# Kernel tuning notes

Measured on AMD Instinct MI355X. Metric: run time of the kernel, lower is better.

The kernel has to match this reference:

```python
import jax, jax.numpy as jnp
import numpy as np

B, S, H, NH = 2, 2048, 1024, 4
DH = H // NH
EPS = 1e-6


def setup_inputs() -> dict:
    key = jax.random.key(0)
    ks = jax.random.split(key, 6)
    q = jax.random.normal(ks[0], (B, S, H), dtype=jnp.float32)
    k = jax.random.normal(ks[1], (B, S, H), dtype=jnp.float32)
    v = jax.random.normal(ks[2], (B, S, H), dtype=jnp.float32)
    # gate projections: Linear(3*H -> NH). Kernels are zero-init in the module;
    # use small random kernels so the projection path is exercised.
    igate_kernel = jax.random.normal(ks[3], (3 * H, NH), dtype=jnp.float32) * 0.02
    fgate_kernel = jax.random.normal(ks[4], (3 * H, NH), dtype=jnp.float32) * 0.02
    igate_bias = jax.random.normal(ks[5], (NH,), dtype=jnp.float32) * 0.1
    fgate_bias = jnp.linspace(3.0, 6.0, NH, dtype=jnp.float32)  # bias_linspace_initializer
    outnorm_scale = jnp.ones((H,), dtype=jnp.float32)  # MultiHeadLayerNorm scale, no bias
    return {"q": q, "k": k, "v": v,
            "igate_kernel": igate_kernel, "igate_bias": igate_bias,
            "fgate_kernel": fgate_kernel, "fgate_bias": fgate_bias,
            "outnorm_scale": outnorm_scale}


def _parallel_stabilized(qh, kh, vh, ig, fg):
    # qh,kh,vh: (B,NH,S,DH); ig,fg: (B,NH,S,1) gate preactivations
    log_fg = jax.nn.log_sigmoid(fg)                      # (B,NH,S,1)
    cs = jnp.cumsum(log_fg, axis=2)                      # cumulative log forget gates
    ltr = jnp.tril(jnp.ones((qh.shape[2], qh.shape[2]), dtype=bool))
    # log decay matrix: sum_{t=j+1}^{i} log f_t = cs[i] - cs[j], masked causal
    log_fg_mat = jnp.where(ltr, cs - jnp.swapaxes(cs, 2, 3), -jnp.inf)  # (B,NH,S,S)
    log_D = log_fg_mat + jnp.swapaxes(ig, 2, 3)          # add input gate per column
    max_log_D = jnp.max(log_D, axis=-1, keepdims=True)   # row-wise stabilizer
    D = jnp.exp(log_D - max_log_D)                       # (B,NH,S,S)
    qk = jnp.einsum("bhsd,bhtd->bhst", qh, kh) / jnp.sqrt(jnp.float32(DH))
    C = qk * D
    normalizer = jnp.maximum(jnp.abs(jnp.sum(C, axis=-1, keepdims=True)),
                             jnp.exp(-max_log_D))
    return jnp.einsum("bhst,bhtd->bhsd", C / (normalizer + EPS), vh)


def reference(q, k, v, igate_kernel, igate_bias, fgate_kernel, fgate_bias, outnorm_scale):
    Bq, Sq, Hq = q.shape
    x = jnp.concatenate([q, k, v], axis=-1)              # (B,S,3H)
    ig = (x @ igate_kernel + igate_bias)                 # (B,S,NH)
    fg = (x @ fgate_kernel + fgate_bias)
    ig = jnp.transpose(ig, (0, 2, 1))[..., None]         # (B,NH,S,1)
    fg = jnp.transpose(fg, (0, 2, 1))[..., None]
    qh = jnp.transpose(q.reshape(Bq, Sq, NH, DH), (0, 2, 1, 3))
    kh = jnp.transpose(k.reshape(Bq, Sq, NH, DH), (0, 2, 1, 3))
    vh = jnp.transpose(v.reshape(Bq, Sq, NH, DH), (0, 2, 1, 3))
    h = _parallel_stabilized(qh, kh, vh, ig, fg)         # (B,NH,S,DH)
    # MultiHeadLayerNorm: per-head layernorm over DH, scale only
    mean = jnp.mean(h, axis=-1, keepdims=True)
    var = jnp.mean((h - mean) ** 2, axis=-1, keepdims=True)
    h_norm = (h - mean) * jax.lax.rsqrt(var + 1e-5)
    h_norm = h_norm * outnorm_scale.reshape(1, NH, 1, DH)
    out = jnp.transpose(h_norm, (0, 2, 1, 3)).reshape(Bq, Sq, Hq)
    return out
```

## Files before the change

### kernel.cpp

```cpp
#include <hip/hip_runtime.h>
#include <hip/hip_bf16.h>


#define S_LEN 2048
#define DHD   256
#define NHEAD 4
#define BATCH 2
#define HID   1024
#define BH_CNT (BATCH*NHEAD)

typedef __attribute__((ext_vector_type(8))) short bf16x8;
typedef __attribute__((ext_vector_type(4))) short short4v;
typedef __attribute__((ext_vector_type(4))) float f32x4;

static __device__ __forceinline__ short f2b(float f) {
  __hip_bfloat16 h = __float2bfloat16(f);
  return *reinterpret_cast<short*>(&h);
}

static __device__ __forceinline__ bf16x8 pack8(f32x4 a, f32x4 b) {
  bf16x8 o;
  o[0]=f2b(a[0]); o[1]=f2b(a[1]); o[2]=f2b(a[2]); o[3]=f2b(a[3]);
  o[4]=f2b(b[0]); o[5]=f2b(b[1]); o[6]=f2b(b[2]); o[7]=f2b(b[3]);
  return o;
}

static __device__ __forceinline__ void gload16(const void* src, void* ldsdst) {
  __builtin_amdgcn_global_load_lds(
      (const __attribute__((address_space(1))) void*)src,
      (__attribute__((address_space(3))) void*)ldsdst, 16, 0, 0);
}

__global__ __launch_bounds__(256) void prep_kernel(
    const float* __restrict__ q, const float* __restrict__ k, const float* __restrict__ v,
    const float* __restrict__ wi, const float* __restrict__ wf,
    short* __restrict__ Kg, short* __restrict__ Vg,
    float* __restrict__ igA, float* __restrict__ fgA) {
  __shared__ short vt2[32][264];
  const int bx = blockIdx.x, t = threadIdx.x;
  if (bx < 768) {
    const int w = t >> 6, lane = t & 63;
    const int gw = bx*4 + w;
    const int seg = gw % 3;
    const int rg = gw / 3;
    const float* xp = (seg == 0) ? q : (seg == 1) ? k : v;
    const float* wip = wi + (long)seg*HID*NHEAD;
    const float* wfp = wf + (long)seg*HID*NHEAD;
    f32x4 ai[4], af[4];
#pragma unroll
    for (int r = 0; r < 4; r++) { ai[r] = f32x4{0,0,0,0}; af[r] = f32x4{0,0,0,0}; }
    for (int cb = 0; cb < HID; cb += 64) {
      const int c = cb + lane;
      const f32x4 wiv = *(const f32x4*)(wip + (long)c*NHEAD);
      const f32x4 wfv = *(const f32x4*)(wfp + (long)c*NHEAD);
#pragma unroll
      for (int r = 0; r < 4; r++) {
        const float x = xp[(long)(rg*4 + r)*HID + c];
        ai[r] += x * wiv;
        af[r] += x * wfv;
      }
    }
#pragma unroll
    for (int mk = 32; mk >= 1; mk >>= 1)
#pragma unroll
      for (int r = 0; r < 4; r++)
#pragma unroll
        for (int e = 0; e < 4; e++) {
          ai[r][e] += __shfl_xor(ai[r][e], mk);
          af[r][e] += __shfl_xor(af[r][e], mk);
        }
    if (lane == 0) {
#pragma unroll
      for (int r = 0; r < 4; r++) {
        const long row = rg*4 + r;
#pragma unroll
        for (int e = 0; e < 4; e++) {
          unsafeAtomicAdd(&igA[row*NHEAD + e], ai[r][e]);
          unsafeAtomicAdd(&fgA[row*NHEAD + e], af[r][e]);
        }
      }
    }
  } else if (bx < 2816) {
    const int kb = bx - 768;
    const int g_row = kb*2 + (t >> 7);
    const int col = (t & 127) * 8;
    const long off = (long)g_row*HID + col;
    const f32x4 xk0 = *(const f32x4*)(k + off);
    const f32x4 xk1 = *(const f32x4*)(k + off + 4);
    bf16x8 o = pack8(xk0, xk1);
    const int b = g_row >> 11, s = g_row & (S_LEN-1);
    const int hh = col >> 8, d = col & 255;
    const int bh = b*NHEAD + hh, jt = s >> 5, rr = s & 31;
    *(bf16x8*)(Kg + ((long)bh*64 + jt)*8192 + rr*256 + (d ^ ((rr & 7) << 3))) = o;
  } else {
    const int t2 = bx - 2816;
    const int jt = t2 & 63, bhv = t2 >> 6;
    const int b = bhv >> 2, hh = bhv & 3;
    const int j0 = jt * 32;
    const int r0 = t >> 3, c0 = (t & 7) * 32;
    const float* vsrc = v + ((long)(b*S_LEN + j0 + r0))*HID + hh*DHD + c0;
#pragma unroll
    for (int i = 0; i < 4; i++) {
      f32x4 a  = *(const f32x4*)(vsrc + i*8);
      f32x4 bb = *(const f32x4*)(vsrc + i*8 + 4);
      *(bf16x8*)&vt2[r0][c0 + i*8] = pack8(a, bb);
    }
    __syncthreads();
    const long base = ((long)bhv*64 + jt) * 8192;
    const int j = t & 31, dg = t >> 5;
#pragma unroll
    for (int dd = 0; dd < 32; dd++) {
      const int d = dg*32 + dd;
      Vg[base + (long)d*32 + (j ^ (((d >> 1) & 3) << 3))] = vt2[j][d];
    }
  }
}

__global__ void scan_kernel(const float* __restrict__ ig, const float* __restrict__ fg,
                            const float* __restrict__ bi, const float* __restrict__ bf_,
                            float* __restrict__ a_out, float* __restrict__ m_out,
                            float* __restrict__ nf_out) {
  int bh = blockIdx.x, b = bh >> 2, h = bh & 3;
  int t = threadIdx.x;
  __shared__ float tot[256];
  long gbase = (long)b * S_LEN;
  const float biv = bi[h], bfv = bf_[h];
  float ls[8];
  float run = 0.f;
  for (int e = 0; e < 8; e++) {
    int s = t*8 + e;
    float x = fg[(gbase + s)*NHEAD + h] + bfv;
    float l = fminf(x, 0.f) - log1pf(expf(-fabsf(x)));
    run += l; ls[e] = run;
  }
  tot[t] = run;
  __syncthreads();
  for (int off = 1; off < 256; off <<= 1) {
    float x = tot[t];
    if (t >= off) x += tot[t - off];
    __syncthreads();
    tot[t] = x;
    __syncthreads();
  }
  float offc = (t == 0) ? 0.f : tot[t-1];
  __syncthreads();
  float av[8], am[8], csv[8];
  float runm = -1e30f;
  for (int e = 0; e < 8; e++) {
    int s = t*8 + e;
    float cs = ls[e] + offc;
    csv[e] = cs;
    float a = (ig[(gbase + s)*NHEAD + h] + biv) - cs;
    av[e] = a;
    runm = fmaxf(runm, a);
    am[e] = runm;
  }
  tot[t] = runm;
  __syncthreads();
  for (int off = 1; off < 256; off <<= 1) {
    float x = tot[t];
    if (t >= off) x = fmaxf(x, tot[t - off]);
    __syncthreads();
    tot[t] = x;
    __syncthreads();
  }
  float offm = (t == 0) ? -1e30f : tot[t-1];
  long obase = (long)bh * S_LEN;
  for (int e = 0; e < 8; e++) {
    int s = t*8 + e;
    float mm = fmaxf(am[e], offm);
    a_out[obase + s]  = av[e];
    m_out[obase + s]  = mm;
    nf_out[obase + s] = expf(-(csv[e] + mm));
  }
}

__global__ __launch_bounds__(256, 2) void mlstm_partial_kernel(
    const float* __restrict__ q, const short* __restrict__ Kg, const short* __restrict__ Vg,
    const float* __restrict__ a_arr, const float* __restrict__ m_arr,
    float* __restrict__ outp, float* __restrict__ rsacc) {
  __shared__ alignas(16) short Kst[2][8192];
  __shared__ alignas(16) short Vst[2][8192];
  __shared__ alignas(16) short plds[4][16*36];
  const int w = threadIdx.x >> 6, lane = threadIdx.x & 63;
  const int lr = lane & 15, g = lane >> 4;
  int pi, it, bh;
  if (blockIdx.x < 256) { pi = 0; bh = blockIdx.x & 7; it = 31 - (int)(blockIdx.x >> 3); }
  else { const int j = blockIdx.x - 256; pi = 1; bh = j & 7; it = j >> 3; }
  const int b = bh >> 2, h = bh & 3;
  const int R0 = it*64 + w*16;
  const long arow = (long)bh * S_LEN;
  const int np = it + 1;
  const int dmax = 2*it + (w >> 1) - pi;
  const int pmax = (dmax >= 0) ? (dmax >> 1) : -1;
  const f32x4 zz = {0.f,0.f,0.f,0.f};
  const int sw = (lr & 7) << 3;

  bf16x8 qf[8];
  const float* qsrc = q + ((long)(b*S_LEN + R0 + lr))*HID + h*DHD + g*8;
#pragma unroll
  for (int c8 = 0; c8 < 8; c8++) {
    f32x4 u0 = *(const f32x4*)(qsrc + c8*32);
    f32x4 u1 = *(const f32x4*)(qsrc + c8*32 + 4);
    qf[c8] = pack8(u0, u1);
  }
  float mrow[4];
#pragma unroll
  for (int r = 0; r < 4; r++) mrow[r] = m_arr[arow + R0 + g*4 + r];

  f32x4 oacc[16];
#pragma unroll
  for (int t = 0; t < 16; t++) oacc[t] = zz;
  float rs[4] = {0.f,0.f,0.f,0.f};
  short* myp = plds[w];

  auto STAGE = [&](int pb, int p) {
    const int jts = 2*p + pi;
    const long toff = ((long)bh*64 + jts)*8192 + w*2048 + lane*8;
    short* kdst = &Kst[pb][w*2048];
    short* vdst = &Vst[pb][w*2048];
    const short* ksrc = Kg + toff;
    const short* vsrc = Vg + toff;
#pragma unroll
    for (int u = 0; u < 4; u++) gload16(ksrc + u*512, kdst + u*512);
#pragma unroll
    for (int u = 0; u < 4; u++) gload16(vsrc + u*512, vdst + u*512);
  };

  float aC0, aC1, aN0 = 0.f, aN1 = 0.f;
  STAGE(0, 0);
  { const int j0 = pi*32;
    aC0 = a_arr[arow + j0 + lr]; aC1 = a_arr[arow + j0 + 16 + lr]; }

  for (int p = 0; p < np; ++p) {
    const int pb = p & 1;
    if (p + 1 < np) {
      STAGE(pb ^ 1, p + 1);
      { const int j0 = (2*(p+1) + pi)*32;
        aN0 = a_arr[arow + j0 + lr]; aN1 = a_arr[arow + j0 + 16 + lr]; }
      asm volatile("s_waitcnt vmcnt(8)" ::: "memory");
    } else {
      asm volatile("s_waitcnt vmcnt(0)" ::: "memory");
    }
    __builtin_amdgcn_s_barrier();

    if (p <= pmax) {
      const int j0 = (2*p + pi)*32;
      const short* Kt = &Kst[pb][0];
      const short* Vt = &Vst[pb][0];
      f32x4 s0 = zz, s1 = zz;
      __builtin_amdgcn_s_setprio(1);
#pragma unroll
      for (int c8 = 0; c8 < 8; c8++) {
        const int ko = lr*256 + ((c8*32 + g*8) ^ sw);
        bf16x8 k0 = *(const bf16x8*)&Kt[ko];
        bf16x8 k1 = *(const bf16x8*)&Kt[ko + 4096];
        s0 = __builtin_amdgcn_mfma_f32_16x16x32_bf16(qf[c8], k0, s0, 0, 0, 0);
        s1 = __builtin_amdgcn_mfma_f32_16x16x32_bf16(qf[c8], k1, s1, 0, 0, 0);
      }
      __builtin_amdgcn_s_setprio(0);
      const bool needmask = (j0 + 31 > R0);
#pragma unroll
      for (int r = 0; r < 4; r++) {
        const int i = R0 + g*4 + r;
        float p0 = s0[r] * 0.0625f * __expf(aC0 - mrow[r]);
        float p1 = s1[r] * 0.0625f * __expf(aC1 - mrow[r]);
        if (needmask) {
          if (j0 + lr > i)      p0 = 0.f;
          if (j0 + 16 + lr > i) p1 = 0.f;
        }
        rs[r] += p0 + p1;
        myp[(g*4 + r)*36 + lr]      = f2b(p0);
        myp[(g*4 + r)*36 + 16 + lr] = f2b(p1);
      }
      const short* rp = myp + lr*36 + g*8;
      short4v plo = *(const short4v*)rp;
      short4v phi = *(const short4v*)(rp + 4);
      bf16x8 pa = {plo[0],plo[1],plo[2],plo[3],phi[0],phi[1],phi[2],phi[3]};
      __builtin_amdgcn_s_setprio(1);
#pragma unroll
      for (int t = 0; t < 16; t++) {
        const int d = t*16 + lr;
        const int vo = d*32 + ((g*8) ^ (((d >> 1) & 3) << 3));
        bf16x8 vf = *(const bf16x8*)&Vt[vo];
        oacc[t] = __builtin_amdgcn_mfma_f32_16x16x32_bf16(pa, vf, oacc[t], 0, 0, 0);
      }
      __builtin_amdgcn_s_setprio(0);
    }
    __builtin_amdgcn_s_barrier();
    if (p + 1 < np) { aC0 = aN0; aC1 = aN1; }
  }

#pragma unroll
  for (int r = 0; r < 4; r++)
    for (int mk = 1; mk < 16; mk <<= 1)
      rs[r] += __shfl_xor(rs[r], mk);

#pragma unroll
  for (int r = 0; r < 4; r++) {
    const int i = R0 + g*4 + r;
    float* orow = outp + ((long)(b*S_LEN + i))*HID + h*DHD + lr;
#pragma unroll
    for (int t = 0; t < 16; t++)
      unsafeAtomicAdd(orow + t*16, oacc[t][r]);
    if (lr == 0)
      unsafeAtomicAdd(&rsacc[arow + i], rs[r]);
  }
}

__global__ __launch_bounds__(256) void finalize_kernel(
    float* __restrict__ outp, const float* __restrict__ rsacc,
    const float* __restrict__ nf_arr, const float* __restrict__ lns) {
  const int bi = blockIdx.x;
  const int h = threadIdx.x >> 6, lane = threadIdx.x & 63;
  const int b = bi >> 11, i = bi & (S_LEN-1);
  const int bh = b*NHEAD + h;
  const long roff = (long)bi * HID + (long)h*DHD;
  f32x4 xv = *(const f32x4*)(outp + roff + lane*4);
  const float rsv = rsacc[(long)bh*S_LEN + i];
  const float nfv = nf_arr[(long)bh*S_LEN + i];
  const float inv = 1.f / (fmaxf(fabsf(rsv), nfv) + 1e-6f);
  xv[0]*=inv; xv[1]*=inv; xv[2]*=inv; xv[3]*=inv;
  float sum = xv[0]+xv[1]+xv[2]+xv[3];
  float sq  = xv[0]*xv[0]+xv[1]*xv[1]+xv[2]*xv[2]+xv[3]*xv[3];
  for (int mk = 1; mk < 64; mk <<= 1) {
    sum += __shfl_xor(sum, mk);
    sq  += __shfl_xor(sq,  mk);
  }
  const float mean = sum * (1.f/256.f);
  const float var  = sq * (1.f/256.f) - mean*mean;
  const float rstd = rsqrtf(var + 1e-5f);
  f32x4 sc = *(const f32x4*)(lns + h*DHD + lane*4);
  f32x4 o;
  o[0]=(xv[0]-mean)*rstd*sc[0]; o[1]=(xv[1]-mean)*rstd*sc[1];
  o[2]=(xv[2]-mean)*rstd*sc[2]; o[3]=(xv[3]-mean)*rstd*sc[3];
  *(f32x4*)(outp + roff + lane*4) = o;
}

extern "C" void kernel_launch(void* const* d_in, const int* in_sizes, int n_in,
                              void* d_out, int out_size, void* d_ws, size_t ws_size,
                              hipStream_t stream) {
  const float* q   = (const float*)d_in[0];
  const float* k   = (const float*)d_in[1];
  const float* v   = (const float*)d_in[2];
  const float* wi  = (const float*)d_in[3];
  const float* bi  = (const float*)d_in[4];
  const float* wf  = (const float*)d_in[5];
  const float* bf_ = (const float*)d_in[6];
  const float* lns = (const float*)d_in[7];
  float* outp = (float*)d_out;

  char* ws = (char*)d_ws;
  const long nelem = (long)BH_CNT * S_LEN * DHD;
  short* Kg  = (short*)ws;
  short* Vg  = Kg + nelem;
  float* igA = (float*)(ws + 2*nelem*sizeof(short));
  float* fgA = igA + (long)BATCH*S_LEN*NHEAD;
  float* aA  = fgA + (long)BATCH*S_LEN*NHEAD;
  float* mA  = aA + (long)BH_CNT*S_LEN;
  float* nfA = mA + (long)BH_CNT*S_LEN;
  float* rsA = nfA + (long)BH_CNT*S_LEN;

  hipMemsetAsync(igA, 0, 2 * (size_t)BATCH*S_LEN*NHEAD * sizeof(float), stream);
  hipMemsetAsync(outp, 0, (size_t)out_size * sizeof(float), stream);
  hipMemsetAsync(rsA, 0, (size_t)BH_CNT * S_LEN * sizeof(float), stream);

  prep_kernel<<<3328, 256, 0, stream>>>(q, k, v, wi, wf, Kg, Vg, igA, fgA);
  scan_kernel<<<BH_CNT, 256, 0, stream>>>(igA, fgA, bi, bf_, aA, mA, nfA);
  mlstm_partial_kernel<<<512, 256, 0, stream>>>(q, Kg, Vg, aA, mA, outp, rsA);
  finalize_kernel<<<BATCH*S_LEN, 256, 0, stream>>>(outp, rsA, nfA, lns);
}
```

Baseline: 110.8 us.

## Fuse output normalization into partial attention kernel via last-block ticket

Removes the separate finalize kernel. Each (head, row-tile) pair is covered by two partial blocks, and each block now bumps an atomic ticket counter. Whichever block arrives second applies the normalizer divide and per-head layernorm to its 16 rows per wave in place. This saves one kernel launch and a full extra pass over the output in a separate kernel, but adds tail work to the later-finishing blocks. There is an ordering risk: the ticket is taken by thread 0 without a block barrier before it, so other threads' atomic adds may not be visible yet. The pipeline wait count is also relaxed from 8 to 10 outstanding loads, so the prefetched gate loads are not waited on early.

```diff
diff --git a/kernel.cpp b/kernel.cpp
--- a/kernel.cpp
+++ b/kernel.cpp
@@ -178,10 +178,12 @@
 __global__ __launch_bounds__(256, 2) void mlstm_partial_kernel(
     const float* __restrict__ q, const short* __restrict__ Kg, const short* __restrict__ Vg,
     const float* __restrict__ a_arr, const float* __restrict__ m_arr,
-    float* __restrict__ outp, float* __restrict__ rsacc) {
+    const float* __restrict__ nf_arr, const float* __restrict__ lns,
+    float* __restrict__ outp, float* __restrict__ rsacc, int* __restrict__ ticket) {
   __shared__ alignas(16) short Kst[2][8192];
   __shared__ alignas(16) short Vst[2][8192];
   __shared__ alignas(16) short plds[4][16*36];
+  __shared__ int lastflag;
   const int w = threadIdx.x >> 6, lane = threadIdx.x & 63;
   const int lr = lane & 15, g = lane >> 4;
   int pi, it, bh;
@@ -238,7 +240,7 @@
       STAGE(pb ^ 1, p + 1);
       { const int j0 = (2*(p+1) + pi)*32;
         aN0 = a_arr[arow + j0 + lr]; aN1 = a_arr[arow + j0 + 16 + lr]; }
-      asm volatile("s_waitcnt vmcnt(8)" ::: "memory");
+      asm volatile("s_waitcnt vmcnt(10)" ::: "memory");
     } else {
       asm volatile("s_waitcnt vmcnt(0)" ::: "memory");
     }
@@ -306,35 +308,37 @@
     if (lr == 0)
       unsafeAtomicAdd(&rsacc[arow + i], rs[r]);
   }
-}
-
-__global__ __launch_bounds__(256) void finalize_kernel(
-    float* __restrict__ outp, const float* __restrict__ rsacc,
-    const float* __restrict__ nf_arr, const float* __restrict__ lns) {
-  const int bi = blockIdx.x;
-  const int h = threadIdx.x >> 6, lane = threadIdx.x & 63;
-  const int b = bi >> 11, i = bi & (S_LEN-1);
-  const int bh = b*NHEAD + h;
-  const long roff = (long)bi * HID + (long)h*DHD;
-  f32x4 xv = *(const f32x4*)(outp + roff + lane*4);
-  const float rsv = rsacc[(long)bh*S_LEN + i];
-  const float nfv = nf_arr[(long)bh*S_LEN + i];
-  const float inv = 1.f / (fmaxf(fabsf(rsv), nfv) + 1e-6f);
-  xv[0]*=inv; xv[1]*=inv; xv[2]*=inv; xv[3]*=inv;
-  float sum = xv[0]+xv[1]+xv[2]+xv[3];
-  float sq  = xv[0]*xv[0]+xv[1]*xv[1]+xv[2]*xv[2]+xv[3]*xv[3];
-  for (int mk = 1; mk < 64; mk <<= 1) {
-    sum += __shfl_xor(sum, mk);
-    sq  += __shfl_xor(sq,  mk);
-  }
-  const float mean = sum * (1.f/256.f);
-  const float var  = sq * (1.f/256.f) - mean*mean;
-  const float rstd = rsqrtf(var + 1e-5f);
-  f32x4 sc = *(const f32x4*)(lns + h*DHD + lane*4);
-  f32x4 o;
-  o[0]=(xv[0]-mean)*rstd*sc[0]; o[1]=(xv[1]-mean)*rstd*sc[1];
-  o[2]=(xv[2]-mean)*rstd*sc[2]; o[3]=(xv[3]-mean)*rstd*sc[3];
-  *(f32x4*)(outp + roff + lane*4) = o;
+
+  if (threadIdx.x == 0) {
+    lastflag = __hip_atomic_fetch_add(&ticket[(bh << 5) | it], 1,
+                                      __ATOMIC_ACQ_REL, __HIP_MEMORY_SCOPE_AGENT);
+  }
+  __syncthreads();
+  if (lastflag == 1) {
+    const f32x4 scv = *(const f32x4*)(lns + h*DHD + lane*4);
+    for (int rr = 0; rr < 16; ++rr) {
+      const int i = R0 + rr;
+      const long roff = ((long)(b*S_LEN + i))*HID + h*DHD;
+      f32x4 xv = *(const f32x4*)(outp + roff + lane*4);
+      const float rsv = rsacc[arow + i];
+      const float nfv = nf_arr[arow + i];
+      const float inv = 1.f / (fmaxf(fabsf(rsv), nfv) + 1e-6f);
+      xv[0]*=inv; xv[1]*=inv; xv[2]*=inv; xv[3]*=inv;
+      float sum = xv[0]+xv[1]+xv[2]+xv[3];
+      float sq  = xv[0]*xv[0]+xv[1]*xv[1]+xv[2]*xv[2]+xv[3]*xv[3];
+      for (int mk = 1; mk < 64; mk <<= 1) {
+        sum += __shfl_xor(sum, mk);
+        sq  += __shfl_xor(sq,  mk);
+      }
+      const float mean = sum * (1.f/256.f);
+      const float var  = sq * (1.f/256.f) - mean*mean;
+      const float rstd = rsqrtf(var + 1e-5f);
+      f32x4 o;
+      o[0]=(xv[0]-mean)*rstd*scv[0]; o[1]=(xv[1]-mean)*rstd*scv[1];
+      o[2]=(xv[2]-mean)*rstd*scv[2]; o[3]=(xv[3]-mean)*rstd*scv[3];
+      *(f32x4*)(outp + roff + lane*4) = o;
+    }
+  }
 }
 
 extern "C" void kernel_launch(void* const* d_in, const int* in_sizes, int n_in,
@@ -360,13 +364,14 @@
   float* mA  = aA + (long)BH_CNT*S_LEN;
   float* nfA = mA + (long)BH_CNT*S_LEN;
   float* rsA = nfA + (long)BH_CNT*S_LEN;
+  int*   tkA = (int*)(rsA + (long)BH_CNT*S_LEN);
 
   hipMemsetAsync(igA, 0, 2 * (size_t)BATCH*S_LEN*NHEAD * sizeof(float), stream);
   hipMemsetAsync(outp, 0, (size_t)out_size * sizeof(float), stream);
-  hipMemsetAsync(rsA, 0, (size_t)BH_CNT * S_LEN * sizeof(float), stream);
+  hipMemsetAsync(rsA, 0, (size_t)BH_CNT * S_LEN * sizeof(float) + 256*sizeof(int), stream);
 
   prep_kernel<<<3328, 256, 0, stream>>>(q, k, v, wi, wf, Kg, Vg, igA, fgA);
   scan_kernel<<<BH_CNT, 256, 0, stream>>>(igA, fgA, bi, bf_, aA, mA, nfA);
-  mlstm_partial_kernel<<<512, 256, 0, stream>>>(q, Kg, Vg, aA, mA, outp, rsA);
-  finalize_kernel<<<BATCH*S_LEN, 256, 0, stream>>>(outp, rsA, nfA, lns);
-}
+  mlstm_partial_kernel<<<512, 256, 0, stream>>>(q, Kg, Vg, aA, mA, nfA, lns,
+                                                outp, rsA, tkA);
+}
```

New measurement: 128.5 us. 16.0% more time.

## Single-buffer V tile and raise occupancy to three blocks per CU

Applied to the files above, without the earlier changes.

The V tile in shared memory drops from double to single buffering. The V load for the current step is now issued at the start of each iteration and overlaps the QK^T MFMA phase, with an extra wait and barrier before the PV phase. Together with launch_bounds raised from 2 to 3 blocks per SM, this cuts LDS per block and is meant to allow more resident blocks for latency hiding. The cost is an extra barrier per iteration, V loads that are exposed when the QK phase is short, and tighter register limits that may cause spills given the 64-float accumulator.

```diff
diff --git a/kernel.cpp b/kernel.cpp
--- a/kernel.cpp
+++ b/kernel.cpp
@@ -175,12 +175,12 @@
   }
 }
 
-__global__ __launch_bounds__(256, 2) void mlstm_partial_kernel(
+__global__ __launch_bounds__(256, 3) void mlstm_partial_kernel(
     const float* __restrict__ q, const short* __restrict__ Kg, const short* __restrict__ Vg,
     const float* __restrict__ a_arr, const float* __restrict__ m_arr,
     float* __restrict__ outp, float* __restrict__ rsacc) {
   __shared__ alignas(16) short Kst[2][8192];
-  __shared__ alignas(16) short Vst[2][8192];
+  __shared__ alignas(16) short Vst[8192];
   __shared__ alignas(16) short plds[4][16*36];
   const int w = threadIdx.x >> 6, lane = threadIdx.x & 63;
   const int lr = lane & 15, g = lane >> 4;
@@ -214,40 +214,46 @@
   float rs[4] = {0.f,0.f,0.f,0.f};
   short* myp = plds[w];
 
-  auto STAGE = [&](int pb, int p) {
+  auto STAGE_K = [&](int pb, int p) {
     const int jts = 2*p + pi;
     const long toff = ((long)bh*64 + jts)*8192 + w*2048 + lane*8;
     short* kdst = &Kst[pb][w*2048];
-    short* vdst = &Vst[pb][w*2048];
     const short* ksrc = Kg + toff;
+#pragma unroll
+    for (int u = 0; u < 4; u++) gload16(ksrc + u*512, kdst + u*512);
+  };
+  auto STAGE_V = [&](int p) {
+    const int jts = 2*p + pi;
+    const long toff = ((long)bh*64 + jts)*8192 + w*2048 + lane*8;
+    short* vdst = &Vst[w*2048];
     const short* vsrc = Vg + toff;
-#pragma unroll
-    for (int u = 0; u < 4; u++) gload16(ksrc + u*512, kdst + u*512);
 #pragma unroll
     for (int u = 0; u < 4; u++) gload16(vsrc + u*512, vdst + u*512);
   };
 
   float aC0, aC1, aN0 = 0.f, aN1 = 0.f;
-  STAGE(0, 0);
+  STAGE_K(0, 0);
   { const int j0 = pi*32;
     aC0 = a_arr[arow + j0 + lr]; aC1 = a_arr[arow + j0 + 16 + lr]; }
 
   for (int p = 0; p < np; ++p) {
     const int pb = p & 1;
-    if (p + 1 < np) {
-      STAGE(pb ^ 1, p + 1);
-      { const int j0 = (2*(p+1) + pi)*32;
-        aN0 = a_arr[arow + j0 + lr]; aN1 = a_arr[arow + j0 + 16 + lr]; }
-      asm volatile("s_waitcnt vmcnt(8)" ::: "memory");
-    } else {
-      asm volatile("s_waitcnt vmcnt(0)" ::: "memory");
-    }
+    const bool more = (p + 1 < np);
+    STAGE_V(p);
+    if (more) {
+      STAGE_K(pb ^ 1, p + 1);
+      const int j0 = (2*(p+1) + pi)*32;
+      aN0 = a_arr[arow + j0 + lr]; aN1 = a_arr[arow + j0 + 16 + lr];
+    }
+    if (more) asm volatile("s_waitcnt vmcnt(8)" ::: "memory");
+    else      asm volatile("s_waitcnt vmcnt(4)" ::: "memory");
     __builtin_amdgcn_s_barrier();
 
-    if (p <= pmax) {
+    bf16x8 pa;
+    const bool act = (p <= pmax);
+    if (act) {
       const int j0 = (2*p + pi)*32;
       const short* Kt = &Kst[pb][0];
-      const short* Vt = &Vst[pb][0];
       f32x4 s0 = zz, s1 = zz;
       __builtin_amdgcn_s_setprio(1);
 #pragma unroll
@@ -276,19 +282,25 @@
       const short* rp = myp + lr*36 + g*8;
       short4v plo = *(const short4v*)rp;
       short4v phi = *(const short4v*)(rp + 4);
-      bf16x8 pa = {plo[0],plo[1],plo[2],plo[3],phi[0],phi[1],phi[2],phi[3]};
+      pa = bf16x8{plo[0],plo[1],plo[2],plo[3],phi[0],phi[1],phi[2],phi[3]};
+    }
+    if (more) asm volatile("s_waitcnt vmcnt(4)" ::: "memory");
+    else      asm volatile("s_waitcnt vmcnt(0)" ::: "memory");
+    __builtin_amdgcn_s_barrier();
+
+    if (act) {
       __builtin_amdgcn_s_setprio(1);
 #pragma unroll
       for (int t = 0; t < 16; t++) {
         const int d = t*16 + lr;
         const int vo = d*32 + ((g*8) ^ (((d >> 1) & 3) << 3));
-        bf16x8 vf = *(const bf16x8*)&Vt[vo];
+        bf16x8 vf = *(const bf16x8*)&Vst[vo];
         oacc[t] = __builtin_amdgcn_mfma_f32_16x16x32_bf16(pa, vf, oacc[t], 0, 0, 0);
       }
       __builtin_amdgcn_s_setprio(0);
     }
     __builtin_amdgcn_s_barrier();
-    if (p + 1 < np) { aC0 = aN0; aC1 = aN1; }
+    if (more) { aC0 = aN0; aC1 = aN1; }
   }
 
 #pragma unroll
```

Result: faster. 105.9 us (-4.5%).
